# Kernel optimization log

Hardware: AMD Instinct MI355X
Metric: run time of the kernel (lower is better)

## Reference

```python
import jax, jax.numpy as jnp
import numpy as np

B, DEPTH, E, NH, HD = 32, 12, 768, 12, 64
IMG, PS, GRID = 224, 16, 14
N = GRID * GRID + 1  # 197 tokens incl. cls
EPS = 1e-5


def _rel_index(wh, ww):
    # BEiT relative position index, incl. cls-token rows/cols
    coords = np.stack(np.meshgrid(np.arange(wh), np.arange(ww), indexing='ij'))
    cf = coords.reshape(2, -1)
    rc = (cf[:, :, None] - cf[:, None, :]).transpose(1, 2, 0).astype(np.int64)
    rc[:, :, 0] += wh - 1
    rc[:, :, 1] += ww - 1
    rc[:, :, 0] *= 2 * ww - 1
    nrd = (2 * wh - 1) * (2 * ww - 1) + 3
    idx = np.zeros((wh * ww + 1, wh * ww + 1), dtype=np.int32)
    idx[1:, 1:] = rc.sum(-1)
    idx[0, :] = nrd - 3
    idx[:, 0] = nrd - 2
    idx[0, 0] = nrd - 1
    return jnp.asarray(idx)

REL_IDX = _rel_index(GRID, GRID)  # [197,197] int32 constant


def _ln(x, w, b):
    m = x.mean(-1, keepdims=True)
    v = ((x - m) ** 2).mean(-1, keepdims=True)
    return (x - m) * jax.lax.rsqrt(v + EPS) * w + b


def setup_inputs() -> dict:
    key = jax.random.key(0)
    ks = jax.random.split(key, 8)
    s = 0.02
    rn = lambda k, shape: jax.random.normal(k, shape, jnp.float32) * s
    D = DEPTH
    return {
        'x': jax.random.normal(ks[0], (B, 3, IMG, IMG), jnp.float32),
        'patch_w': rn(ks[1], (E, 3 * PS * PS)),
        'patch_b': jnp.zeros((E,), jnp.float32),
        'cls_token': jnp.zeros((1, 1, E), jnp.float32),
        'ln1_w': jnp.ones((D, E), jnp.float32),
        'ln1_b': jnp.zeros((D, E), jnp.float32),
        'qkv_w': rn(ks[2], (D, 3 * E, E)),
        'q_bias': jnp.zeros((D, E), jnp.float32),
        'v_bias': jnp.zeros((D, E), jnp.float32),
        'rel_table': rn(ks[3], (D, (2 * GRID - 1) ** 2 + 3, NH)),
        'proj_w': rn(ks[4], (D, E, E)),
        'proj_b': jnp.zeros((D, E), jnp.float32),
        'ln2_w': jnp.ones((D, E), jnp.float32),
        'ln2_b': jnp.zeros((D, E), jnp.float32),
        'fc1_w': rn(ks[5], (D, 4 * E, E)),
        'fc1_b': jnp.zeros((D, 4 * E), jnp.float32),
        'fc2_w': rn(ks[6], (D, E, 4 * E)),
        'fc2_b': jnp.zeros((D, E), jnp.float32),
        'fcn_w': jnp.ones((E,), jnp.float32),
        'fcn_b': jnp.zeros((E,), jnp.float32),
        'head_w': rn(ks[7], (1000, E)),
        'head_b': jnp.zeros((1000,), jnp.float32),
    }


def reference(x, patch_w, patch_b, cls_token, ln1_w, ln1_b, qkv_w, q_bias,
              v_bias, rel_table, proj_w, proj_b, ln2_w, ln2_b, fc1_w, fc1_b,
              fc2_w, fc2_b, fcn_w, fcn_b, head_w, head_b):
    b = x.shape[0]
    scale = HD ** -0.5
    # patch embed: stride-16 conv == patchify + matmul (weight flattened as [E, C*kh*kw])
    patches = x.reshape(b, 3, GRID, PS, GRID, PS).transpose(0, 2, 4, 1, 3, 5)
    patches = patches.reshape(b, GRID * GRID, 3 * PS * PS)
    tok = patches @ patch_w.T + patch_b
    tok = jnp.concatenate([jnp.broadcast_to(cls_token, (b, 1, E)), tok], axis=1)  # [B,197,E]

    params = dict(ln1_w=ln1_w, ln1_b=ln1_b, qkv_w=qkv_w, q_bias=q_bias,
                  v_bias=v_bias, rel_table=rel_table, proj_w=proj_w,
                  proj_b=proj_b, ln2_w=ln2_w, ln2_b=ln2_b, fc1_w=fc1_w,
                  fc1_b=fc1_b, fc2_w=fc2_w, fc2_b=fc2_b)

    def block(h, p):
        y = _ln(h, p['ln1_w'], p['ln1_b'])
        qkvb = jnp.concatenate([p['q_bias'], jnp.zeros_like(p['q_bias']), p['v_bias']])
        qkv = (y @ p['qkv_w'].T + qkvb).reshape(b, N, 3, NH, HD).transpose(2, 0, 3, 1, 4)
        q, k, v = qkv[0] * scale, qkv[1], qkv[2]  # [B,H,N,hd]
        bias = p['rel_table'][REL_IDX].transpose(2, 0, 1)  # [H,N,N]
        att = jax.nn.softmax(jnp.einsum('bhnd,bhmd->bhnm', q, k) + bias[None], axis=-1)
        o = jnp.einsum('bhnm,bhmd->bhnd', att, v).transpose(0, 2, 1, 3).reshape(b, N, E)
        h = h + o @ p['proj_w'].T + p['proj_b']
        y = _ln(h, p['ln2_w'], p['ln2_b'])
        y = jax.nn.gelu(y @ p['fc1_w'].T + p['fc1_b'], approximate=False)
        return h + y @ p['fc2_w'].T + p['fc2_b'], None

    tok, _ = jax.lax.scan(block, tok, params)
    feat = _ln(tok[:, 1:].mean(axis=1), fcn_w, fcn_b)  # mean pooling over patch tokens
    return feat @ head_w.T + head_b  # [B, 1000]
```

## Files before the change

kernel.cpp:

```cpp
#include <hip/hip_runtime.h>
#include <hip/hip_bf16.h>
#include <math.h>


typedef __hip_bfloat16 bf16;
using short8 = __attribute__((ext_vector_type(8))) short;
using f32x4  = __attribute__((ext_vector_type(4))) float;

#define NTOK 197
#define NHEAD 12
#define NPAD 224

#define S_QKV  1769472
#define S_PROJ 589824
#define S_FC   2359296
#define O_PROJ 1769472
#define O_FC1  2359296
#define O_FC2  4718592
#define W_TOT  7077888

#define GLD(gp, lp) __builtin_amdgcn_global_load_lds( \
    (const unsigned int __attribute__((address_space(1)))*)(gp), \
    (unsigned int __attribute__((address_space(3)))*)(lp), 16, 0, 0)

__global__ __launch_bounds__(256) void cvt_k(const float* __restrict__ src,
                                             bf16* __restrict__ dst, int n8) {
  int t = blockIdx.x * 256 + threadIdx.x;
  if (t >= n8) return;
  size_t i = (size_t)t * 8;
  float4 a = *(const float4*)(src + i);
  float4 b = *(const float4*)(src + i + 4);
  union { short8 v; bf16 e[8]; } u;
  u.e[0] = __float2bfloat16(a.x); u.e[1] = __float2bfloat16(a.y);
  u.e[2] = __float2bfloat16(a.z); u.e[3] = __float2bfloat16(a.w);
  u.e[4] = __float2bfloat16(b.x); u.e[5] = __float2bfloat16(b.y);
  u.e[6] = __float2bfloat16(b.z); u.e[7] = __float2bfloat16(b.w);
  *(short8*)(dst + i) = u.v;
}

__device__ __forceinline__ int ridx(int n, int m) {
  if (n == 0) return (m == 0) ? 731 : 729;
  if (m == 0) return 730;
  int nh = (n - 1) / 14, nw = (n - 1) % 14;
  int mh = (m - 1) / 14, mw = (m - 1) % 14;
  return (nh - mh + 13) * 27 + (nw - mw + 13);
}

__global__ __launch_bounds__(256) void prep_k(
    const float* __restrict__ qkvw, const float* __restrict__ projw,
    const float* __restrict__ fc1w, const float* __restrict__ fc2w,
    const float* __restrict__ rel, bf16* __restrict__ wl,
    float* __restrict__ biasT, int d) {
  int blk = blockIdx.x;
  if (blk < 3456) {
    size_t i = ((size_t)blk * 256 + threadIdx.x) * 8;
    const float* src;
    if (i < O_PROJ)      src = qkvw + (size_t)d * S_QKV + i;
    else if (i < O_FC1)  src = projw + (size_t)d * S_PROJ + (i - O_PROJ);
    else if (i < O_FC2)  src = fc1w + (size_t)d * S_FC + (i - O_FC1);
    else                 src = fc2w + (size_t)d * S_FC + (i - O_FC2);
    float4 a = *(const float4*)src;
    float4 b = *(const float4*)(src + 4);
    union { short8 v; bf16 e[8]; } u;
    u.e[0] = __float2bfloat16(a.x); u.e[1] = __float2bfloat16(a.y);
    u.e[2] = __float2bfloat16(a.z); u.e[3] = __float2bfloat16(a.w);
    u.e[4] = __float2bfloat16(b.x); u.e[5] = __float2bfloat16(b.y);
    u.e[6] = __float2bfloat16(b.z); u.e[7] = __float2bfloat16(b.w);
    *(short8*)(wl + i) = u.v;
  } else {
    int idx = (blk - 3456) * 256 + threadIdx.x;
    int h = idx / (NPAD * 256);
    int rem = idx % (NPAD * 256);
    int m = rem / 256, n = rem % 256;
    float v;
    if (m >= NTOK) {
      v = -1e30f;
    } else {
      int nn = min(n, NTOK - 1);
      v = rel[((size_t)d * 732 + ridx(nn, m)) * 12 + h];
    }
    biasT[idx] = v;
  }
}

__global__ __launch_bounds__(256) void patchify_k(const float* __restrict__ x,
                                                  bf16* __restrict__ patches) {
  int o = blockIdx.x * 256 + threadIdx.x;
  if (o >= 6272 * 768) return;
  int row = o / 768, col = o % 768;
  int b = row / 196, g = row % 196;
  int gh = g / 14, gw = g % 14;
  int c = col / 256, r = col % 256;
  int ph = r / 16, pw = r % 16;
  patches[o] = __float2bfloat16(
      x[(((size_t)b * 3 + c) * 224 + gh * 16 + ph) * 224 + gw * 16 + pw]);
}

__global__ __launch_bounds__(256) void clsfill_k(const float* __restrict__ cls,
                                                 float* __restrict__ h) {
  int i = blockIdx.x * 256 + threadIdx.x;
  if (i >= 32 * 768) return;
  int b = i / 768, e = i % 768;
  h[((size_t)b * 197) * 768 + e] = cls[e];
}

__global__ __launch_bounds__(256) void vtz_k(bf16* __restrict__ vt) {
  int i = blockIdx.x * 256 + threadIdx.x;
  if (i >= 32 * 12 * 64 * NPAD / 8) return;
  *(short8*)(vt + (size_t)i * 8) = (short8){0,0,0,0,0,0,0,0};
}

template <int EPI>
__global__ __launch_bounds__(512, 4) void mm256_k(
    const bf16* __restrict__ A, const bf16* __restrict__ W,
    const float* __restrict__ bias, const float* __restrict__ bias2,
    void* __restrict__ Cout, bf16* __restrict__ vtg,
    int M, int Nn, int K) {
  constexpr int BUFSZ = 24576;
  __shared__ __attribute__((aligned(16))) char lds[3 * BUFSZ];
  const int tid = threadIdx.x;
  const int lane = tid & 63, wave = tid >> 6;
  const int wr = wave >> 1, wc = wave & 1;
  const int l15 = lane & 15, lg = lane >> 4;
  const int row0 = blockIdx.x * 256, n0 = blockIdx.y * 128;
  const int nt = K >> 5, ntm1 = nt - 1;

  const bf16 *gA0, *gA1, *gB0;
  int dA0, dA1, dB0;
  {
    int s = tid * 16;
    int r = s >> 6, cl = ((s >> 4) & 3) ^ ((r >> 1) & 3);
    gA0 = A + (size_t)(row0 + r) * K + cl * 8;  dA0 = s;
    s = 8192 + tid * 16;
    r = s >> 6; cl = ((s >> 4) & 3) ^ ((r >> 1) & 3);
    gA1 = A + (size_t)(row0 + r) * K + cl * 8;  dA1 = s;
    s = tid * 16;
    r = s >> 6; cl = ((s >> 4) & 3) ^ ((r >> 1) & 3);
    gB0 = W + (size_t)(n0 + r) * K + cl * 8;    dB0 = 16384 + s;
  }
  int oA[4], oB[4];
#pragma unroll
  for (int m = 0; m < 4; m++) {
    int r = wr * 64 + m * 16 + l15;
    oA[m] = (r << 6) | ((lg ^ ((r >> 1) & 3)) << 4);
  }
#pragma unroll
  for (int n = 0; n < 4; n++) {
    int r = wc * 64 + n * 16 + l15;
    oB[n] = 16384 + ((r << 6) | ((lg ^ ((r >> 1) & 3)) << 4));
  }

  f32x4 acc[4][4];
#pragma unroll
  for (int m = 0; m < 4; m++)
#pragma unroll
    for (int n = 0; n < 4; n++) acc[m][n] = (f32x4){0.f, 0.f, 0.f, 0.f};

  GLD(gA0, lds + dA0); GLD(gA1, lds + dA1); GLD(gB0, lds + dB0);
  GLD(gA0 + 32, lds + BUFSZ + dA0); GLD(gA1 + 32, lds + BUFSZ + dA1);
  GLD(gB0 + 32, lds + BUFSZ + dB0);
  asm volatile("s_waitcnt vmcnt(3)" ::: "memory");
  __builtin_amdgcn_s_barrier();
  __builtin_amdgcn_sched_barrier(0);

#define MB(RB, WB, tt)                                                        \
  {                                                                           \
    int ks = (tt) + 2; if (ks > ntm1) ks = ntm1; ks <<= 5;                    \
    char* wb = lds + (WB) * BUFSZ;                                            \
    GLD(gA0 + ks, wb + dA0); GLD(gA1 + ks, wb + dA1);                         \
    GLD(gB0 + ks, wb + dB0);                                                  \
    const char* rb = lds + (RB) * BUFSZ;                                      \
    short8 a[4], b[4];                                                        \
    _Pragma("unroll") for (int m = 0; m < 4; m++)                             \
      a[m] = *(const short8*)(rb + oA[m]);                                    \
    _Pragma("unroll") for (int n = 0; n < 4; n++)                             \
      b[n] = *(const short8*)(rb + oB[n]);                                    \
    __builtin_amdgcn_s_setprio(1);                                            \
    _Pragma("unroll") for (int m = 0; m < 4; m++)                             \
      _Pragma("unroll") for (int n = 0; n < 4; n++)                           \
        acc[m][n] = __builtin_amdgcn_mfma_f32_16x16x32_bf16(a[m], b[n], acc[m][n], 0, 0, 0); \
    __builtin_amdgcn_s_setprio(0);                                            \
    __builtin_amdgcn_sched_barrier(0);                                        \
    asm volatile("s_waitcnt vmcnt(2)" ::: "memory");                          \
    __builtin_amdgcn_s_barrier();                                             \
    __builtin_amdgcn_sched_barrier(0);                                        \
  }

  for (int t = 0; t < nt; t += 3) {
    MB(0, 2, t); MB(1, 0, t + 1); MB(2, 1, t + 2);
  }
#undef MB
  asm volatile("s_waitcnt vmcnt(0)" ::: "memory");

#pragma unroll
  for (int m = 0; m < 4; m++) {
    const int rbase = row0 + wr * 64 + m * 16 + lg * 4;
#pragma unroll
    for (int n = 0; n < 4; n++) {
      const int gc = n0 + wc * 64 + n * 16 + l15;
      f32x4 v = acc[m][n];
#pragma unroll
      for (int j = 0; j < 4; j++) {
        int gr = rbase + j;
        if (gr >= M) continue;
        float val = v[j];
        if (EPI == 1) {
          if (gc < 768) val += bias[gc];
          else if (gc >= 1536) val += bias2[gc - 1536];
          if (gc >= 1536) {
            int ob = gr / 197, nn = gr - ob * 197, hd = gc - 1536;
            vtg[(((size_t)ob * 12 + (hd >> 6)) * 64 + (hd & 63)) * NPAD + nn] =
                __float2bfloat16(val);
          } else {
            ((bf16*)Cout)[(size_t)gr * Nn + gc] = __float2bfloat16(val);
          }
        } else {
          val += bias[gc];
          val = 0.5f * val * (1.f + erff(val * 0.70710678118654752f));
          ((bf16*)Cout)[(size_t)gr * Nn + gc] = __float2bfloat16(val);
        }
      }
    }
  }
}

template <int EPI>
__global__ __launch_bounds__(256, 3) void mm128_k(
    const bf16* __restrict__ A, const bf16* __restrict__ W,
    const float* __restrict__ bias, const float* __restrict__ Res,
    void* __restrict__ Cout, int M, int Nn, int K) {
  constexpr int BUFSZ = 16384;
  __shared__ __attribute__((aligned(16))) char lds[3 * BUFSZ];
  const int tid = threadIdx.x;
  const int lane = tid & 63, wave = tid >> 6;
  const int wr = wave >> 1, wc = wave & 1;
  const int l15 = lane & 15, lg = lane >> 4;
  const int row0 = blockIdx.x * 128, n0 = blockIdx.y * 128;
  const int nt = K >> 5, ntm1 = nt - 1;

  const bf16 *gA0, *gA1, *gB0, *gB1;
  int dA0, dA1, dB0, dB1;
  {
    int s = tid * 16;
    int r = s >> 6, cl = ((s >> 4) & 3) ^ ((r >> 1) & 3);
    gA0 = A + (size_t)(row0 + r) * K + cl * 8;  dA0 = s;
    s = 4096 + tid * 16;
    r = s >> 6; cl = ((s >> 4) & 3) ^ ((r >> 1) & 3);
    gA1 = A + (size_t)(row0 + r) * K + cl * 8;  dA1 = s;
    s = tid * 16;
    r = s >> 6; cl = ((s >> 4) & 3) ^ ((r >> 1) & 3);
    gB0 = W + (size_t)(n0 + r) * K + cl * 8;    dB0 = 8192 + s;
    s = 4096 + tid * 16;
    r = s >> 6; cl = ((s >> 4) & 3) ^ ((r >> 1) & 3);
    gB1 = W + (size_t)(n0 + r) * K + cl * 8;    dB1 = 8192 + s;
  }
  int oA[4], oB[4];
#pragma unroll
  for (int m = 0; m < 4; m++) {
    int r = wr * 64 + m * 16 + l15;
    oA[m] = (r << 6) | ((lg ^ ((r >> 1) & 3)) << 4);
  }
#pragma unroll
  for (int n = 0; n < 4; n++) {
    int r = wc * 64 + n * 16 + l15;
    oB[n] = 8192 + ((r << 6) | ((lg ^ ((r >> 1) & 3)) << 4));
  }

  f32x4 acc[4][4];
#pragma unroll
  for (int m = 0; m < 4; m++)
#pragma unroll
    for (int n = 0; n < 4; n++) acc[m][n] = (f32x4){0.f, 0.f, 0.f, 0.f};

  GLD(gA0, lds + dA0); GLD(gA1, lds + dA1);
  GLD(gB0, lds + dB0); GLD(gB1, lds + dB1);
  GLD(gA0 + 32, lds + BUFSZ + dA0); GLD(gA1 + 32, lds + BUFSZ + dA1);
  GLD(gB0 + 32, lds + BUFSZ + dB0); GLD(gB1 + 32, lds + BUFSZ + dB1);
  asm volatile("s_waitcnt vmcnt(4)" ::: "memory");
  __builtin_amdgcn_s_barrier();
  __builtin_amdgcn_sched_barrier(0);

#define MB(RB, WB, tt)                                                        \
  {                                                                           \
    int ks = (tt) + 2; if (ks > ntm1) ks = ntm1; ks <<= 5;                    \
    char* wb = lds + (WB) * BUFSZ;                                            \
    GLD(gA0 + ks, wb + dA0); GLD(gA1 + ks, wb + dA1);                         \
    GLD(gB0 + ks, wb + dB0); GLD(gB1 + ks, wb + dB1);                         \
    const char* rb = lds + (RB) * BUFSZ;                                      \
    short8 a[4], b[4];                                                        \
    _Pragma("unroll") for (int m = 0; m < 4; m++)                             \
      a[m] = *(const short8*)(rb + oA[m]);                                    \
    _Pragma("unroll") for (int n = 0; n < 4; n++)                             \
      b[n] = *(const short8*)(rb + oB[n]);                                    \
    __builtin_amdgcn_s_setprio(1);                                            \
    _Pragma("unroll") for (int m = 0; m < 4; m++)                             \
      _Pragma("unroll") for (int n = 0; n < 4; n++)                           \
        acc[m][n] = __builtin_amdgcn_mfma_f32_16x16x32_bf16(a[m], b[n], acc[m][n], 0, 0, 0); \
    __builtin_amdgcn_s_setprio(0);                                            \
    __builtin_amdgcn_sched_barrier(0);                                        \
    asm volatile("s_waitcnt vmcnt(3)" ::: "memory");                          \
    __builtin_amdgcn_s_barrier();                                             \
    __builtin_amdgcn_sched_barrier(0);                                        \
  }

  for (int t = 0; t < nt; t += 3) {
    MB(0, 2, t); MB(1, 0, t + 1); MB(2, 1, t + 2);
  }
#undef MB
  asm volatile("s_waitcnt vmcnt(0)" ::: "memory");

#pragma unroll
  for (int m = 0; m < 4; m++) {
    const int rbase = row0 + wr * 64 + m * 16 + lg * 4;
#pragma unroll
    for (int n = 0; n < 4; n++) {
      const int gc = n0 + wc * 64 + n * 16 + l15;
      f32x4 v = acc[m][n];
#pragma unroll
      for (int j = 0; j < 4; j++) {
        int gr = rbase + j;
        if (gr >= M) continue;
        float val = v[j] + bias[gc];
        if (EPI == 2) val += Res[(size_t)gr * Nn + gc];
        int orow = (EPI == 0) ? (gr + gr / 196 + 1) : gr;
        ((float*)Cout)[(size_t)orow * Nn + gc] = val;
      }
    }
  }
}

__global__ __launch_bounds__(256) void ln_k(const float* __restrict__ in,
                                            bf16* __restrict__ outp,
                                            const float* __restrict__ w,
                                            const float* __restrict__ b,
                                            int rows) {
  int row = blockIdx.x * 4 + threadIdx.y;
  if (row >= rows) return;
  int lane = threadIdx.x;
  const float4* xr = (const float4*)(in + (size_t)row * 768);
  float4 v[3];
  float s = 0.f;
#pragma unroll
  for (int i = 0; i < 3; i++) {
    v[i] = xr[lane + i * 64];
    s += (v[i].x + v[i].y) + (v[i].z + v[i].w);
  }
#pragma unroll
  for (int o = 32; o; o >>= 1) s += __shfl_xor(s, o);
  float mean = s * (1.f / 768.f);
  float var = 0.f;
#pragma unroll
  for (int i = 0; i < 3; i++) {
    float d0 = v[i].x - mean, d1 = v[i].y - mean;
    float d2 = v[i].z - mean, d3 = v[i].w - mean;
    var += (d0 * d0 + d1 * d1) + (d2 * d2 + d3 * d3);
  }
#pragma unroll
  for (int o = 32; o; o >>= 1) var += __shfl_xor(var, o);
  float rs = rsqrtf(var * (1.f / 768.f) + 1e-5f);
  const float4* w4 = (const float4*)w;
  const float4* b4 = (const float4*)b;
  bf16* orow = outp + (size_t)row * 768;
#pragma unroll
  for (int i = 0; i < 3; i++) {
    int e4 = lane + i * 64;
    float4 wv = w4[e4], bv = b4[e4];
    union { bf16 h; short s; } c0, c1, c2, c3;
    c0.h = __float2bfloat16((v[i].x - mean) * rs * wv.x + bv.x);
    c1.h = __float2bfloat16((v[i].y - mean) * rs * wv.y + bv.y);
    c2.h = __float2bfloat16((v[i].z - mean) * rs * wv.z + bv.z);
    c3.h = __float2bfloat16((v[i].w - mean) * rs * wv.w + bv.w);
    short4 o4 = make_short4(c0.s, c1.s, c2.s, c3.s);
    *(short4*)(orow + e4 * 4) = o4;
  }
}

__device__ __forceinline__ unsigned pkbf(float a, float b) {
  union { bf16 h; unsigned short u; } ua, ub;
  ua.h = __float2bfloat16(a); ub.h = __float2bfloat16(b);
  return ((unsigned)ub.u << 16) | (unsigned)ua.u;
}

__global__ __launch_bounds__(256) void attn2_k(const bf16* __restrict__ qkvb,
                                               const bf16* __restrict__ vtg,
                                               const float* __restrict__ biasT,
                                               bf16* __restrict__ outp) {
  __shared__ bf16 Ks[NPAD * 64];
  __shared__ bf16 Vt[64 * NPAD];
  __shared__ bf16 Ps[4][64 * 32];
  __shared__ float denl[4][64];

  const int bh = blockIdx.x;
  const int b = bh / 12, h = bh % 12;
  const int tid = threadIdx.x;
  const int wave = tid >> 6, lane = tid & 63;
  const int l15 = lane & 15, lg = lane >> 4;
  const int qbase = wave * 64;

  const bf16* vsrc = vtg + (size_t)bh * 64 * NPAD;
#pragma unroll
  for (int i = 0; i < 7; i++) {
    int c = i * 256 + tid;
    GLD(vsrc + c * 8, Vt + c * 8);
  }
#pragma unroll
  for (int i = 0; i < 7; i++) {
    int slot = i * 256 + tid;
    int r = slot >> 3, c8 = (slot & 7) * 8;
    int rg = min(r, NTOK - 1);
    short8 kv = *(const short8*)(qkvb + (size_t)(b * NTOK + rg) * 2304 + 768 + h * 64 + c8);
    int byte = (r * 128 + c8 * 2) ^ ((r & 7) << 4);
    *(short8*)((char*)Ks + byte) = kv;
  }
  short8 qf[4][2];
#pragma unroll
  for (int nf = 0; nf < 4; nf++) {
    int n = qbase + nf * 16 + l15;
    const bf16* qp = qkvb + (size_t)(b * NTOK + min(n, NTOK - 1)) * 2304 + h * 64;
    qf[nf][0] = *(const short8*)(qp + lg * 8);
    qf[nf][1] = *(const short8*)(qp + 32 + lg * 8);
  }
  __syncthreads();

  f32x4 Oacc[4][4];
#pragma unroll
  for (int i = 0; i < 4; i++)
#pragma unroll
    for (int j = 0; j < 4; j++) Oacc[i][j] = (f32x4){0.f, 0.f, 0.f, 0.f};
  float den[4] = {0.f, 0.f, 0.f, 0.f};
  const float* bT = biasT + (size_t)h * NPAD * 256;
  char* pw = (char*)&Ps[wave][0];

  for (int c = 0; c < 7; c++) {
    const int m0 = c * 32;
    f32x4 st[2][4];
#pragma unroll
    for (int mf = 0; mf < 2; mf++)
#pragma unroll
      for (int nf = 0; nf < 4; nf++) st[mf][nf] = (f32x4){0.f, 0.f, 0.f, 0.f};
#pragma unroll
    for (int kk = 0; kk < 2; kk++) {
      short8 af[2];
#pragma unroll
      for (int mf = 0; mf < 2; mf++) {
        int m = m0 + mf * 16 + l15;
        int byte = (m * 128 + kk * 64 + lg * 16) ^ ((m & 7) << 4);
        af[mf] = *(const short8*)((const char*)Ks + byte);
      }
#pragma unroll
      for (int mf = 0; mf < 2; mf++)
#pragma unroll
        for (int nf = 0; nf < 4; nf++)
          st[mf][nf] = __builtin_amdgcn_mfma_f32_16x16x32_bf16(af[mf], qf[nf][kk], st[mf][nf], 0, 0, 0);
    }
#pragma unroll
    for (int mf = 0; mf < 2; mf++) {
      int mrow = m0 + mf * 16 + lg * 4;
#pragma unroll
      for (int nf = 0; nf < 4; nf++) {
        int n = qbase + nf * 16 + l15;
        float p0 = __expf(st[mf][nf][0] * 0.125f + bT[(mrow + 0) * 256 + n]);
        float p1 = __expf(st[mf][nf][1] * 0.125f + bT[(mrow + 1) * 256 + n]);
        float p2 = __expf(st[mf][nf][2] * 0.125f + bT[(mrow + 2) * 256 + n]);
        float p3 = __expf(st[mf][nf][3] * 0.125f + bT[(mrow + 3) * 256 + n]);
        den[nf] += (p0 + p1) + (p2 + p3);
        int nl = nf * 16 + l15;
        int byte = (nl * 64 + (mf * 16 + lg * 4) * 2) ^ ((nl & 7) << 4);
        *(unsigned*)(pw + byte) = pkbf(p0, p1);
        *(unsigned*)(pw + byte + 4) = pkbf(p2, p3);
      }
    }
    short8 pa[4], vb[4];
#pragma unroll
    for (int nf = 0; nf < 4; nf++) {
      int nl = nf * 16 + l15;
      int byte = (nl * 64 + lg * 16) ^ ((nl & 7) << 4);
      pa[nf] = *(const short8*)((const char*)pw + byte);
    }
#pragma unroll
    for (int df = 0; df < 4; df++) {
      int d = df * 16 + l15;
      vb[df] = *(const short8*)(Vt + d * NPAD + m0 + lg * 8);
    }
#pragma unroll
    for (int nf = 0; nf < 4; nf++)
#pragma unroll
      for (int df = 0; df < 4; df++)
        Oacc[nf][df] = __builtin_amdgcn_mfma_f32_16x16x32_bf16(pa[nf], vb[df], Oacc[nf][df], 0, 0, 0);
  }

#pragma unroll
  for (int nf = 0; nf < 4; nf++) {
    den[nf] += __shfl_xor(den[nf], 16);
    den[nf] += __shfl_xor(den[nf], 32);
    denl[wave][nf * 16 + l15] = den[nf];
  }
  float inv[4][4];
#pragma unroll
  for (int nf = 0; nf < 4; nf++)
#pragma unroll
    for (int j = 0; j < 4; j++)
      inv[nf][j] = 1.f / denl[wave][nf * 16 + lg * 4 + j];
#pragma unroll
  for (int nf = 0; nf < 4; nf++) {
#pragma unroll
    for (int df = 0; df < 4; df++) {
#pragma unroll
      for (int j = 0; j < 4; j++) {
        int n = qbase + nf * 16 + lg * 4 + j;
        if (n < NTOK)
          outp[(size_t)(b * NTOK + n) * 768 + h * 64 + df * 16 + l15] =
              __float2bfloat16(Oacc[nf][df][j] * inv[nf][j]);
      }
    }
  }
}

__device__ __forceinline__ float block_sum(float v, float* sm4) {
#pragma unroll
  for (int o = 32; o; o >>= 1) v += __shfl_down(v, o);
  __syncthreads();
  if ((threadIdx.x & 63) == 0) sm4[threadIdx.x >> 6] = v;
  __syncthreads();
  return sm4[0] + sm4[1] + sm4[2] + sm4[3];
}

__global__ __launch_bounds__(256) void pool_ln_k(const float* __restrict__ h,
                                                 const float* __restrict__ w,
                                                 const float* __restrict__ bi,
                                                 float* __restrict__ feat) {
  __shared__ float sm4[4];
  int b = blockIdx.x, tid = threadIdx.x;
  float vals[3];
  float local = 0.f;
#pragma unroll
  for (int j = 0; j < 3; j++) {
    int e = tid + j * 256;
    float s = 0.f;
    for (int nn = 1; nn < 197; nn++) s += h[((size_t)(b * 197 + nn)) * 768 + e];
    s *= (1.f / 196.f);
    vals[j] = s;
    local += s;
  }
  float tot = block_sum(local, sm4);
  float mean = tot * (1.f / 768.f);
  float lv = 0.f;
#pragma unroll
  for (int j = 0; j < 3; j++) { float d = vals[j] - mean; lv += d * d; }
  float vtot = block_sum(lv, sm4);
  float rs = rsqrtf(vtot * (1.f / 768.f) + 1e-5f);
#pragma unroll
  for (int j = 0; j < 3; j++) {
    int e = tid + j * 256;
    feat[(size_t)b * 768 + e] = (vals[j] - mean) * rs * w[e] + bi[e];
  }
}

__global__ __launch_bounds__(256) void head_k(const float* __restrict__ A,
                                              const float* __restrict__ W,
                                              const float* __restrict__ bias,
                                              float* __restrict__ C,
                                              int M, int Nn, int K) {
  __shared__ float As[16][64 + 4];
  __shared__ float Bs[16][64 + 4];
  int tid = threadIdx.x;
  int tx = tid & 15, ty = tid >> 4;
  int row0 = blockIdx.x * 64, n0 = blockIdx.y * 64;
  int lrow = tid >> 2;
  int kq = (tid & 3) * 4;
  float acc[4][4];
#pragma unroll
  for (int i = 0; i < 4; i++)
#pragma unroll
    for (int j = 0; j < 4; j++) acc[i][j] = 0.f;
  for (int k0 = 0; k0 < K; k0 += 16) {
    float4 av = make_float4(0.f, 0.f, 0.f, 0.f);
    if (row0 + lrow < M) av = *(const float4*)&A[(size_t)(row0 + lrow) * K + k0 + kq];
    As[kq + 0][lrow] = av.x; As[kq + 1][lrow] = av.y;
    As[kq + 2][lrow] = av.z; As[kq + 3][lrow] = av.w;
    float4 bv = make_float4(0.f, 0.f, 0.f, 0.f);
    if (n0 + lrow < Nn) bv = *(const float4*)&W[(size_t)(n0 + lrow) * K + k0 + kq];
    Bs[kq + 0][lrow] = bv.x; Bs[kq + 1][lrow] = bv.y;
    Bs[kq + 2][lrow] = bv.z; Bs[kq + 3][lrow] = bv.w;
    __syncthreads();
#pragma unroll
    for (int kk = 0; kk < 16; kk++) {
      float4 a = *(const float4*)&As[kk][ty * 4];
      float4 b = *(const float4*)&Bs[kk][tx * 4];
      float aa[4] = {a.x, a.y, a.z, a.w};
      float bb[4] = {b.x, b.y, b.z, b.w};
#pragma unroll
      for (int i = 0; i < 4; i++)
#pragma unroll
        for (int j = 0; j < 4; j++) acc[i][j] = fmaf(aa[i], bb[j], acc[i][j]);
    }
    __syncthreads();
  }
#pragma unroll
  for (int i = 0; i < 4; i++) {
    int gr = row0 + ty * 4 + i;
    if (gr >= M) continue;
#pragma unroll
    for (int j = 0; j < 4; j++) {
      int gc = n0 + tx * 4 + j;
      if (gc >= Nn) continue;
      C[(size_t)gr * Nn + gc] = acc[i][j] + bias[gc];
    }
  }
}

extern "C" void kernel_launch(void* const* d_in, const int* in_sizes, int n_in,
                              void* d_out, int out_size, void* d_ws, size_t ws_size,
                              hipStream_t stream) {
  const float* x       = (const float*)d_in[0];
  const float* patch_w = (const float*)d_in[1];
  const float* patch_b = (const float*)d_in[2];
  const float* cls_tok = (const float*)d_in[3];
  const float* ln1_w   = (const float*)d_in[4];
  const float* ln1_b   = (const float*)d_in[5];
  const float* qkv_w   = (const float*)d_in[6];
  const float* q_bias  = (const float*)d_in[7];
  const float* v_bias  = (const float*)d_in[8];
  const float* rel_tab = (const float*)d_in[9];
  const float* proj_w  = (const float*)d_in[10];
  const float* proj_b  = (const float*)d_in[11];
  const float* ln2_w   = (const float*)d_in[12];
  const float* ln2_b   = (const float*)d_in[13];
  const float* fc1_w   = (const float*)d_in[14];
  const float* fc1_b   = (const float*)d_in[15];
  const float* fc2_w   = (const float*)d_in[16];
  const float* fc2_b   = (const float*)d_in[17];
  const float* fcn_w   = (const float*)d_in[18];
  const float* fcn_b   = (const float*)d_in[19];
  const float* head_w  = (const float*)d_in[20];
  const float* head_b  = (const float*)d_in[21];
  float* outp = (float*)d_out;

  char* wsb = (char*)d_ws;
  float* h    = (float*)wsb;  wsb += 19365888;
  bf16* bigb  = (bf16*)wsb;   wsb += 29048832;
  bf16* yb    = (bf16*)wsb;   wsb += 9830400;
  bf16* hid   = (bf16*)wsb;   wsb += 39321600;
  bf16* wl    = (bf16*)wsb;   wsb += 14155776;
  bf16* vt_g  = (bf16*)wsb;   wsb += 11010048;
  float* biasT = (float*)wsb; wsb += 2752512;
  float* feat = (float*)wsb;

  const int M = 6304;

  vtz_k<<<2688, 256, 0, stream>>>(vt_g);
  patchify_k<<<(6272 * 768 + 255) / 256, 256, 0, stream>>>(x, hid);
  cvt_k<<<(589824 / 8 + 255) / 256, 256, 0, stream>>>(patch_w, wl, 589824 / 8);
  mm128_k<0><<<dim3(49, 6), 256, 0, stream>>>(
      hid, wl, patch_b, nullptr, h, 6272, 768, 768);
  clsfill_k<<<(32 * 768 + 255) / 256, 256, 0, stream>>>(cls_tok, h);

  for (int d = 0; d < 12; d++) {
    prep_k<<<6144, 256, 0, stream>>>(qkv_w, proj_w, fc1_w, fc2_w, rel_tab,
                                     wl, biasT, d);
    ln_k<<<dim3((M + 3) / 4), dim3(64, 4), 0, stream>>>(h, yb, ln1_w + d * 768, ln1_b + d * 768, M);
    mm256_k<1><<<dim3(25, 18), 512, 0, stream>>>(
        yb, wl, q_bias + d * 768, v_bias + d * 768, bigb, vt_g, M, 2304, 768);
    attn2_k<<<32 * NHEAD, 256, 0, stream>>>(bigb, vt_g, biasT, yb);
    mm128_k<2><<<dim3(50, 6), 256, 0, stream>>>(
        yb, wl + O_PROJ, proj_b + d * 768, h, h, M, 768, 768);
    ln_k<<<dim3((M + 3) / 4), dim3(64, 4), 0, stream>>>(h, yb, ln2_w + d * 768, ln2_b + d * 768, M);
    mm256_k<3><<<dim3(25, 24), 512, 0, stream>>>(
        yb, wl + O_FC1, fc1_b + d * 3072, nullptr, hid, nullptr, M, 3072, 768);
    mm128_k<2><<<dim3(50, 6), 256, 0, stream>>>(
        hid, wl + O_FC2, fc2_b + d * 768, h, h, M, 768, 3072);
  }

  pool_ln_k<<<32, 256, 0, stream>>>(h, fcn_w, fcn_b, feat);
  {
    dim3 g(1, (1000 + 63) / 64);
    head_k<<<g, 256, 0, stream>>>(feat, head_w, head_b, outp, 32, 1000, 768);
  }
}
```

Measured before the change: 3.299 ms.

## Enlarge QKV/FC1 GEMM tile to 256x256 with two-phase double-buffered loads

Replaces the 256x128 triple-buffered GEMM used for the QKV and FC1 projections with a 256x256 tile. Each K step is split into two phases: the first computes half the A rows while loading the second half of the next tile. The layout becomes a 2x4 wave grid with 8x4 accumulators per wave. The goal is to raise data reuse per LDS byte and cut global traffic per FLOP. The costs are more accumulator registers, lower occupancy (launch bounds 2), and half as many blocks (225/300), which may leave CUs idle on a 256-CU part.

Measured after the change: 3.974 ms. 1.2x slower.

```diff
diff --git a/kernel.cpp b/kernel.cpp
--- a/kernel.cpp
+++ b/kernel.cpp
@@ -111,37 +111,36 @@
 }
 
 template <int EPI>
-__global__ __launch_bounds__(512, 4) void mm256_k(
+__global__ __launch_bounds__(512, 2) void mm2ph_k(
     const bf16* __restrict__ A, const bf16* __restrict__ W,
     const float* __restrict__ bias, const float* __restrict__ bias2,
     void* __restrict__ Cout, bf16* __restrict__ vtg,
     int M, int Nn, int K) {
-  constexpr int BUFSZ = 24576;
-  __shared__ __attribute__((aligned(16))) char lds[3 * BUFSZ];
+  constexpr int BUFSZ = 32768;
+  __shared__ __attribute__((aligned(16))) char lds[2 * BUFSZ];
   const int tid = threadIdx.x;
   const int lane = tid & 63, wave = tid >> 6;
-  const int wr = wave >> 1, wc = wave & 1;
+  const int wr = wave >> 2;
+  const int wc = wave & 3;
   const int l15 = lane & 15, lg = lane >> 4;
-  const int row0 = blockIdx.x * 256, n0 = blockIdx.y * 128;
+  const int row0 = blockIdx.x * 256, n0 = blockIdx.y * 256;
   const int nt = K >> 5, ntm1 = nt - 1;
 
-  const bf16 *gA0, *gA1, *gB0;
-  int dA0, dA1, dB0;
+  const bf16 *gA0h, *gA1h, *gB0h, *gB1h;
+  int dA0h, dA1h, dB0h, dB1h;
   {
     int s = tid * 16;
-    int r = s >> 6, cl = ((s >> 4) & 3) ^ ((r >> 1) & 3);
-    gA0 = A + (size_t)(row0 + r) * K + cl * 8;  dA0 = s;
-    s = 8192 + tid * 16;
-    r = s >> 6; cl = ((s >> 4) & 3) ^ ((r >> 1) & 3);
-    gA1 = A + (size_t)(row0 + r) * K + cl * 8;  dA1 = s;
-    s = tid * 16;
-    r = s >> 6; cl = ((s >> 4) & 3) ^ ((r >> 1) & 3);
-    gB0 = W + (size_t)(n0 + r) * K + cl * 8;    dB0 = 16384 + s;
-  }
-  int oA[4], oB[4];
-#pragma unroll
-  for (int m = 0; m < 4; m++) {
-    int r = wr * 64 + m * 16 + l15;
+    int lr = s >> 6;
+    int cl = ((s >> 4) & 3) ^ ((lr >> 1) & 3);
+    gA0h = A + (size_t)(row0 + lr) * K + cl * 8;        dA0h = s;
+    gA1h = A + (size_t)(row0 + 128 + lr) * K + cl * 8;  dA1h = 8192 + s;
+    gB0h = W + (size_t)(n0 + lr) * K + cl * 8;          dB0h = 16384 + s;
+    gB1h = W + (size_t)(n0 + 128 + lr) * K + cl * 8;    dB1h = 24576 + s;
+  }
+  int oA[8], oB[4];
+#pragma unroll
+  for (int m = 0; m < 8; m++) {
+    int r = wr * 128 + m * 16 + l15;
     oA[m] = (r << 6) | ((lg ^ ((r >> 1) & 3)) << 4);
   }
 #pragma unroll
@@ -150,51 +149,59 @@
     oB[n] = 16384 + ((r << 6) | ((lg ^ ((r >> 1) & 3)) << 4));
   }
 
-  f32x4 acc[4][4];
-#pragma unroll
-  for (int m = 0; m < 4; m++)
+  f32x4 acc[8][4];
+#pragma unroll
+  for (int m = 0; m < 8; m++)
 #pragma unroll
     for (int n = 0; n < 4; n++) acc[m][n] = (f32x4){0.f, 0.f, 0.f, 0.f};
 
-  GLD(gA0, lds + dA0); GLD(gA1, lds + dA1); GLD(gB0, lds + dB0);
-  GLD(gA0 + 32, lds + BUFSZ + dA0); GLD(gA1 + 32, lds + BUFSZ + dA1);
-  GLD(gB0 + 32, lds + BUFSZ + dB0);
-  asm volatile("s_waitcnt vmcnt(3)" ::: "memory");
-  __builtin_amdgcn_s_barrier();
-  __builtin_amdgcn_sched_barrier(0);
-
-#define MB(RB, WB, tt)                                                        \
-  {                                                                           \
-    int ks = (tt) + 2; if (ks > ntm1) ks = ntm1; ks <<= 5;                    \
-    char* wb = lds + (WB) * BUFSZ;                                            \
-    GLD(gA0 + ks, wb + dA0); GLD(gA1 + ks, wb + dA1);                         \
-    GLD(gB0 + ks, wb + dB0);                                                  \
-    const char* rb = lds + (RB) * BUFSZ;                                      \
-    short8 a[4], b[4];                                                        \
-    _Pragma("unroll") for (int m = 0; m < 4; m++)                             \
-      a[m] = *(const short8*)(rb + oA[m]);                                    \
-    _Pragma("unroll") for (int n = 0; n < 4; n++)                             \
-      b[n] = *(const short8*)(rb + oB[n]);                                    \
-    __builtin_amdgcn_s_setprio(1);                                            \
-    _Pragma("unroll") for (int m = 0; m < 4; m++)                             \
-      _Pragma("unroll") for (int n = 0; n < 4; n++)                           \
-        acc[m][n] = __builtin_amdgcn_mfma_f32_16x16x32_bf16(a[m], b[n], acc[m][n], 0, 0, 0); \
-    __builtin_amdgcn_s_setprio(0);                                            \
-    __builtin_amdgcn_sched_barrier(0);                                        \
-    asm volatile("s_waitcnt vmcnt(2)" ::: "memory");                          \
-    __builtin_amdgcn_s_barrier();                                             \
-    __builtin_amdgcn_sched_barrier(0);                                        \
-  }
-
-  for (int t = 0; t < nt; t += 3) {
-    MB(0, 2, t); MB(1, 0, t + 1); MB(2, 1, t + 2);
-  }
-#undef MB
+  GLD(gA0h, lds + dA0h); GLD(gA1h, lds + dA1h);
+  GLD(gB0h, lds + dB0h); GLD(gB1h, lds + dB1h);
+
+  for (int t = 0; t < nt; ++t) {
+    const int p = t & 1;
+    const char* rb = lds + p * BUFSZ;
+    char* wb = lds + (p ^ 1) * BUFSZ;
+    const int ks = ((t + 1 <= ntm1) ? (t + 1) : ntm1) << 5;
+    GLD(gA0h + ks, wb + dA0h);
+    GLD(gB0h + ks, wb + dB0h);
+    asm volatile("s_waitcnt vmcnt(2)" ::: "memory");
+    __builtin_amdgcn_s_barrier();
+    __builtin_amdgcn_sched_barrier(0);
+    short8 b[4], a[4];
+#pragma unroll
+    for (int n = 0; n < 4; n++) b[n] = *(const short8*)(rb + oB[n]);
+#pragma unroll
+    for (int m = 0; m < 4; m++) a[m] = *(const short8*)(rb + oA[m]);
+    __builtin_amdgcn_s_setprio(1);
+#pragma unroll
+    for (int m = 0; m < 4; m++)
+#pragma unroll
+      for (int n = 0; n < 4; n++)
+        acc[m][n] = __builtin_amdgcn_mfma_f32_16x16x32_bf16(a[m], b[n], acc[m][n], 0, 0, 0);
+    __builtin_amdgcn_s_setprio(0);
+    __builtin_amdgcn_sched_barrier(0);
+    __builtin_amdgcn_s_barrier();
+    GLD(gA1h + ks, wb + dA1h);
+    GLD(gB1h + ks, wb + dB1h);
+    short8 a2[4];
+#pragma unroll
+    for (int m = 0; m < 4; m++) a2[m] = *(const short8*)(rb + oA[4 + m]);
+    __builtin_amdgcn_s_setprio(1);
+#pragma unroll
+    for (int m = 0; m < 4; m++)
+#pragma unroll
+      for (int n = 0; n < 4; n++)
+        acc[4 + m][n] = __builtin_amdgcn_mfma_f32_16x16x32_bf16(a2[m], b[n], acc[4 + m][n], 0, 0, 0);
+    __builtin_amdgcn_s_setprio(0);
+    __builtin_amdgcn_sched_barrier(0);
+    __builtin_amdgcn_s_barrier();
+  }
   asm volatile("s_waitcnt vmcnt(0)" ::: "memory");
 
 #pragma unroll
-  for (int m = 0; m < 4; m++) {
-    const int rbase = row0 + wr * 64 + m * 16 + lg * 4;
+  for (int m = 0; m < 8; m++) {
+    const int rbase = row0 + wr * 128 + m * 16 + lg * 4;
 #pragma unroll
     for (int n = 0; n < 4; n++) {
       const int gc = n0 + wc * 64 + n * 16 + l15;
@@ -659,13 +666,13 @@
     prep_k<<<6144, 256, 0, stream>>>(qkv_w, proj_w, fc1_w, fc2_w, rel_tab,
                                      wl, biasT, d);
     ln_k<<<dim3((M + 3) / 4), dim3(64, 4), 0, stream>>>(h, yb, ln1_w + d * 768, ln1_b + d * 768, M);
-    mm256_k<1><<<dim3(25, 18), 512, 0, stream>>>(
+    mm2ph_k<1><<<dim3(25, 9), 512, 0, stream>>>(
         yb, wl, q_bias + d * 768, v_bias + d * 768, bigb, vt_g, M, 2304, 768);
     attn2_k<<<32 * NHEAD, 256, 0, stream>>>(bigb, vt_g, biasT, yb);
     mm128_k<2><<<dim3(50, 6), 256, 0, stream>>>(
         yb, wl + O_PROJ, proj_b + d * 768, h, h, M, 768, 768);
     ln_k<<<dim3((M + 3) / 4), dim3(64, 4), 0, stream>>>(h, yb, ln2_w + d * 768, ln2_b + d * 768, M);
-    mm256_k<3><<<dim3(25, 24), 512, 0, stream>>>(
+    mm2ph_k<3><<<dim3(25, 12), 512, 0, stream>>>(
         yb, wl + O_FC1, fc1_b + d * 3072, nullptr, hid, nullptr, M, 3072, 768);
     mm128_k<2><<<dim3(50, 6), 256, 0, stream>>>(
         hid, wl + O_FC2, fc2_b + d * 768, h, h, M, 768, 3072);
```
